# Optimization experiments

Hardware: AMD Instinct MI355X
Metric: run time of the kernel (lower is better)

Reference implementation:

```python
import jax, jax.numpy as jnp
import numpy as np

N = 20000
NEG_SLOPE = 0.2


def gat_conv(x, src, dst, W, att_src, att_dst, bias, heads, ch, concat):
    # x: [N, F_in]; src/dst: [E] (messages flow src -> dst, softmax grouped by dst)
    n = x.shape[0]
    h = (x @ W).reshape(n, heads, ch)                      # [N, H, C]
    a_s = jnp.sum(h * att_src, axis=-1)                    # [N, H]
    a_d = jnp.sum(h * att_dst, axis=-1)                    # [N, H]
    e = jax.nn.leaky_relu(a_s[src] + a_d[dst], NEG_SLOPE)  # [E, H]
    m = jax.ops.segment_max(e, dst, num_segments=n)        # segment-softmax (stable)
    ex = jnp.exp(e - m[dst])
    denom = jax.ops.segment_sum(ex, dst, num_segments=n)
    alpha = ex / (denom[dst] + 1e-16)                      # [E, H]
    msg = h[src] * alpha[:, :, None]                       # [E, H, C]
    out = jax.ops.segment_sum(msg, dst, num_segments=n)    # [N, H, C]
    out = out.reshape(n, heads * ch) if concat else out.mean(axis=1)
    return out + bias


def setup_inputs() -> dict:
    key = jax.random.key(0)
    ks = jax.random.split(key, 24)
    in_ch, h_ch, out_ch, H, OH = 512, 128, 64, 4, 6
    hid = H * h_ch  # 512
    s = 0.1
    d = {
        "x": jax.random.normal(ks[0], (N, in_ch), jnp.float32),
        "edge_index": jax.random.randint(ks[1], (2, 160000), 0, N, jnp.int32),
        "W1": jax.random.normal(ks[2], (in_ch, H * h_ch), jnp.float32) * s,
        "as1": jax.random.normal(ks[3], (1, H, h_ch), jnp.float32) * s,
        "ad1": jax.random.normal(ks[4], (1, H, h_ch), jnp.float32) * s,
        "b1": jnp.zeros((H * h_ch,), jnp.float32),
        "lW1": jax.random.normal(ks[5], (in_ch, hid), jnp.float32) * s,
        "lb1": jnp.zeros((hid,), jnp.float32),
        "W2": jax.random.normal(ks[6], (hid, H * h_ch), jnp.float32) * s,
        "as2": jax.random.normal(ks[7], (1, H, h_ch), jnp.float32) * s,
        "ad2": jax.random.normal(ks[8], (1, H, h_ch), jnp.float32) * s,
        "b2": jnp.zeros((H * h_ch,), jnp.float32),
        "lW2": jax.random.normal(ks[9], (hid, hid), jnp.float32) * s,
        "lb2": jnp.zeros((hid,), jnp.float32),
        "W3": jax.random.normal(ks[10], (hid, OH * out_ch), jnp.float32) * s,
        "as3": jax.random.normal(ks[11], (1, OH, out_ch), jnp.float32) * s,
        "ad3": jax.random.normal(ks[12], (1, OH, out_ch), jnp.float32) * s,
        "b3": jnp.zeros((out_ch,), jnp.float32),
        "lW3": jax.random.normal(ks[13], (hid, out_ch), jnp.float32) * s,
        "lb3": jnp.zeros((out_ch,), jnp.float32),
    }
    return d


def reference(x, edge_index, W1, as1, ad1, b1, lW1, lb1,
              W2, as2, ad2, b2, lW2, lb2,
              W3, as3, ad3, b3, lW3, lb3):
    n = x.shape[0]
    loops = jnp.arange(n, dtype=edge_index.dtype)  # PyG GATConv add_self_loops=True
    src = jnp.concatenate([edge_index[0], loops])
    dst = jnp.concatenate([edge_index[1], loops])
    h = jax.nn.elu(gat_conv(x, src, dst, W1, as1, ad1, b1, 4, 128, True) + x @ lW1 + lb1)
    h = jax.nn.elu(gat_conv(h, src, dst, W2, as2, ad2, b2, 4, 128, True) + h @ lW2 + lb2)
    out = gat_conv(h, src, dst, W3, as3, ad3, b3, 6, 64, False) + h @ lW3 + lb3
    return out
```

## Files before the change

### kernel.cpp

```cpp
#include <hip/hip_runtime.h>
#include <cstddef>
#include <cstdint>
#include <type_traits>

#define N_NODES 20000
#define NPAD 20096
#define E0_EDGES 160000
#define E_TOT (E0_EDGES + N_NODES)
#define CAP 64

typedef __bf16 bf16x8 __attribute__((ext_vector_type(8)));
typedef float f32x4 __attribute__((ext_vector_type(4)));

__device__ __forceinline__ ushort f2bf(float f) {
  uint32_t u = __float_as_uint(f);
  return (ushort)((u + 0x7FFFu + ((u >> 16) & 1u)) >> 16);
}
__device__ __forceinline__ float bf2f(ushort h) {
  return __uint_as_float((uint32_t)h << 16);
}

__device__ __forceinline__ int SW(int r) { return ((r >> 1) & 3) ^ ((r >> 3) & 1); }

#define GLOAD16(g, l)                                                         \
  __builtin_amdgcn_global_load_lds(                                           \
      (const __attribute__((address_space(1))) void*)(uintptr_t)(g),          \
      (__attribute__((address_space(3))) void*)(uint32_t)(uintptr_t)(l),      \
      16, 0, 0)


__global__ void fill_csr_kernel(const int* __restrict__ ei, int* __restrict__ cnt,
                                int* __restrict__ slots) {
  int e = blockIdx.x * blockDim.x + threadIdx.x;
  if (e >= E_TOT) return;
  int src, dst;
  if (e < E0_EDGES) { src = ei[e]; dst = ei[E0_EDGES + e]; }
  else              { src = e - E0_EDGES; dst = src; }
  int pos = atomicAdd(&cnt[dst], 1);
  if (pos < CAP) slots[dst * CAP + pos] = src;
}


__global__ void convert_x_kernel(const float* __restrict__ x, ushort* __restrict__ xb) {
  size_t i = ((size_t)blockIdx.x * blockDim.x + threadIdx.x) * 4;
  if (i >= (size_t)NPAD * 512) return;
  if (i < (size_t)N_NODES * 512) {
    float4 v = *(const float4*)(x + i);
    ushort4 o;
    o.x = f2bf(v.x); o.y = f2bf(v.y); o.z = f2bf(v.z); o.w = f2bf(v.w);
    *(ushort4*)(xb + i) = o;
  } else {
    *(ushort4*)(xb + i) = make_ushort4(0, 0, 0, 0);
  }
}

__global__ void transpose_all_kernel(
    const float* __restrict__ W1, const float* __restrict__ lW1,
    const float* __restrict__ W2, const float* __restrict__ lW2,
    const float* __restrict__ W3, const float* __restrict__ lW3,
    ushort* __restrict__ Bt1, ushort* __restrict__ Bt2, ushort* __restrict__ Bt3) {
  __shared__ float tile[32][33];
  const int K = 512;
  int z = blockIdx.z;
  const float* W; ushort* B; int M;
  switch (z) {
    case 0:  W = W1;  B = Bt1;              M = 512; break;
    case 1:  W = lW1; B = Bt1 + 512 * 512;  M = 512; break;
    case 2:  W = W2;  B = Bt2;              M = 512; break;
    case 3:  W = lW2; B = Bt2 + 512 * 512;  M = 512; break;
    case 4:  W = W3;  B = Bt3;              M = 384; break;
    default: W = lW3; B = Bt3 + 384 * 512;  M = 64;  break;
  }
  int mb = blockIdx.x * 32, kb = blockIdx.y * 32;
  if (mb >= M) return;
  int tx = threadIdx.x, ty = threadIdx.y;
#pragma unroll
  for (int i = 0; i < 32; i += 8)
    tile[ty + i][tx] = W[(size_t)(kb + ty + i) * M + mb + tx];
  __syncthreads();
#pragma unroll
  for (int i = 0; i < 32; i += 8)
    B[(size_t)(mb + ty + i) * K + kb + tx] = f2bf(tile[tx][ty + i]);
}


template <typename Out1T>
__global__ __launch_bounds__(256, 3) void mfma_gemm_kernel(
    const ushort* __restrict__ A,
    const ushort* __restrict__ Bt,
    ushort* __restrict__ out0, int ld0, int split,
    Out1T* __restrict__ out1, int ld1, int Mout1, const float* __restrict__ bias1,
    const float* __restrict__ att_sw, const float* __restrict__ att_dw,
    float* __restrict__ a_sp, float* __restrict__ a_dp,
    int nheads, int headC,
    int NT, int nwg) {
  const int K = 512;
  __shared__ __attribute__((aligned(16))) ushort As[3][128][32];
  __shared__ __attribute__((aligned(16))) ushort Bs[3][128][32];

  int tid = threadIdx.x, lane = tid & 63, wave = tid >> 6;
  int wrow = (wave >> 1) * 64, wcol = (wave & 1) * 64;

  size_t K2 = (size_t)K * 2;
  int rofs = lane >> 2;
  int gch = (lane & 3) ^ SW(rofs);
  int srow[2];
#pragma unroll
  for (int it = 0; it < 2; ++it) srow[it] = wave * 32 + it * 16;

  int fr = lane & 15, hi = lane >> 4;
  int rch = hi ^ SW(fr);

  char* AsB = (char*)&As[0][0][0];
  char* BsB = (char*)&Bs[0][0][0];

  int q = nwg >> 3, r = nwg & 7;

  for (int w0 = blockIdx.x; w0 < nwg; w0 += gridDim.x) {
    int xcd = w0 & 7, pos = w0 >> 3;
    int wgid = (xcd < r ? xcd * (q + 1) : r * (q + 1) + (xcd - r) * q) + pos;
    int by = wgid / NT, bx = wgid - by * NT;
    int bm = by * 128, bn = bx * 128;

    const char* pA[2];
    const char* pB[2];
#pragma unroll
    for (int it = 0; it < 2; ++it) {
      pA[it] = (const char*)A + (size_t)(bm + srow[it] + rofs) * K2 + gch * 16;
      pB[it] = (const char*)Bt + (size_t)(bn + srow[it] + rofs) * K2 + gch * 16;
    }

    f32x4 acc[4][4] = {};

#pragma unroll
    for (int s = 0; s < 2; ++s) {
#pragma unroll
      for (int it = 0; it < 2; ++it) {
        GLOAD16(pA[it], AsB + s * 8192 + srow[it] * 64);
        GLOAD16(pB[it], BsB + s * 8192 + srow[it] * 64);
      }
#pragma unroll
      for (int it = 0; it < 2; ++it) { pA[it] += 64; pB[it] += 64; }
    }

    for (int k = 0; k < 16; ++k) {
      if (k + 1 < 16) asm volatile("s_waitcnt vmcnt(4) lgkmcnt(0)" ::: "memory");
      else            asm volatile("s_waitcnt vmcnt(0) lgkmcnt(0)" ::: "memory");
      __builtin_amdgcn_s_barrier();
      asm volatile("" ::: "memory");
      if (k + 2 < 16) {
        int ss = (k + 2) % 3;
#pragma unroll
        for (int it = 0; it < 2; ++it) {
          GLOAD16(pA[it], AsB + ss * 8192 + srow[it] * 64);
          GLOAD16(pB[it], BsB + ss * 8192 + srow[it] * 64);
        }
#pragma unroll
        for (int it = 0; it < 2; ++it) { pA[it] += 64; pB[it] += 64; }
      }
      {
        int sc = k % 3;
        bf16x8 af[4], bf[4];
#pragma unroll
        for (int i = 0; i < 4; ++i)
          af[i] = *(const bf16x8*)&As[sc][wrow + i * 16 + fr][rch * 8];
#pragma unroll
        for (int j = 0; j < 4; ++j)
          bf[j] = *(const bf16x8*)&Bs[sc][wcol + j * 16 + fr][rch * 8];
#pragma unroll
        for (int i = 0; i < 4; ++i)
#pragma unroll
          for (int j = 0; j < 4; ++j)
            acc[i][j] = __builtin_amdgcn_mfma_f32_16x16x32_bf16(af[i], bf[j], acc[i][j], 0, 0, 0);
      }
      asm volatile("" ::: "memory");
    }

    asm volatile("s_waitcnt lgkmcnt(0)" ::: "memory");
    __builtin_amdgcn_s_barrier();
    asm volatile("" ::: "memory");

    int colg = bn + wcol;
    bool lower = colg < split;
    int g4 = hi << 2;
    int ccol = fr;
#pragma unroll
    for (int i = 0; i < 4; ++i) {
#pragma unroll
      for (int rr = 0; rr < 4; ++rr) {
        int row = bm + wrow + g4 + i * 16 + rr;
        if (row >= N_NODES) continue;
#pragma unroll
        for (int j = 0; j < 4; ++j) {
          int col = colg + j * 16 + ccol;
          float v = acc[i][j][rr];
          if (lower) {
            out0[(size_t)row * ld0 + col] = f2bf(v);
          } else {
            int c1 = col - split;
            if (c1 < Mout1) {
              float b = v + bias1[c1];
              if constexpr (std::is_same<Out1T, ushort>::value)
                out1[(size_t)row * ld1 + c1] = f2bf(b);
              else
                out1[(size_t)row * ld1 + c1] = b;
            }
          }
        }
      }
    }

    if (lower) {
      int hd = colg / headC;
      int cb = colg - hd * headC;
      int half = (cb >> 6) & 1;
      float ws4[4], wd4[4];
#pragma unroll
      for (int j = 0; j < 4; ++j) {
        int cc = hd * headC + cb + j * 16 + ccol;
        ws4[j] = att_sw[cc];
        wd4[j] = att_dw[cc];
      }
#pragma unroll
      for (int i = 0; i < 4; ++i) {
#pragma unroll
        for (int rr = 0; rr < 4; ++rr) {
          float ps = 0.f, pd = 0.f;
#pragma unroll
          for (int j = 0; j < 4; ++j) { ps += acc[i][j][rr] * ws4[j]; pd += acc[i][j][rr] * wd4[j]; }
#pragma unroll
          for (int o = 1; o < 16; o <<= 1) { ps += __shfl_xor(ps, o); pd += __shfl_xor(pd, o); }
          if ((lane & 15) == 0) {
            int row = bm + wrow + g4 + i * 16 + rr;
            if (row < N_NODES) {
              size_t idx = ((size_t)row * nheads + hd) * 2;
              if (headC == 128) {
                a_sp[idx + half] = ps;
                a_dp[idx + half] = pd;
              } else {
                a_sp[idx] = ps;  a_sp[idx + 1] = 0.f;
                a_dp[idx] = pd;  a_dp[idx + 1] = 0.f;
              }
            }
          }
        }
      }
    }
  }
}


template <int H, int C>
__global__ __launch_bounds__(128) void gather12_fused(
    const int* __restrict__ cnt, const int* __restrict__ slots,
    const float* __restrict__ a_sp, const float* __restrict__ a_dp,
    const ushort* __restrict__ hbuf, const float* __restrict__ gat_bias,
    const ushort* __restrict__ skip_in, ushort* __restrict__ outbuf) {
  __shared__ float al[H][CAP];
  __shared__ int srcs[CAP];
  int n = blockIdx.x;
  int t = threadIdx.x, lane = t & 63, w = t >> 6;
  int deg = min(cnt[n], CAP);

  int sj = 0;
  if (lane < deg) sj = slots[n * CAP + lane];
#pragma unroll
  for (int hh = 0; hh < 2; ++hh) {
    int hd = 2 * w + hh;
    float e = -1e30f;
    if (lane < deg) {
      size_t is = ((size_t)sj * H + hd) * 2;
      size_t id = ((size_t)n * H + hd) * 2;
      float v = a_sp[is] + a_sp[is + 1] + a_dp[id] + a_dp[id + 1];
      e = v > 0.f ? v : 0.2f * v;
    }
    float m = e;
#pragma unroll
    for (int o = 32; o > 0; o >>= 1) m = fmaxf(m, __shfl_xor(m, o));
    float ex = (lane < deg) ? expf(e - m) : 0.f;
    float s = ex;
#pragma unroll
    for (int o = 32; o > 0; o >>= 1) s += __shfl_xor(s, o);
    float inv = 1.f / (s + 1e-16f);
    if (lane < deg) al[hd][lane] = ex * inv;
  }
  if (w == 0 && lane < deg) srcs[lane] = sj;
  __syncthreads();

  int f0 = 4 * t, hd = t >> 5;
  float a0 = 0.f, a1 = 0.f, a2 = 0.f, a3 = 0.f;
  for (int j = 0; j < deg; ++j) {
    float a = al[hd][j];
    ushort4 hv = *(const ushort4*)(hbuf + (size_t)srcs[j] * (H * C) + f0);
    a0 += a * bf2f(hv.x);
    a1 += a * bf2f(hv.y);
    a2 += a * bf2f(hv.z);
    a3 += a * bf2f(hv.w);
  }
  ushort4 sk = *(const ushort4*)(skip_in + (size_t)n * (H * C) + f0);
  float o0 = a0 + gat_bias[f0 + 0] + bf2f(sk.x);
  float o1 = a1 + gat_bias[f0 + 1] + bf2f(sk.y);
  float o2 = a2 + gat_bias[f0 + 2] + bf2f(sk.z);
  float o3 = a3 + gat_bias[f0 + 3] + bf2f(sk.w);
  o0 = o0 > 0.f ? o0 : (expf(o0) - 1.f);
  o1 = o1 > 0.f ? o1 : (expf(o1) - 1.f);
  o2 = o2 > 0.f ? o2 : (expf(o2) - 1.f);
  o3 = o3 > 0.f ? o3 : (expf(o3) - 1.f);
  ushort4 ov;
  ov.x = f2bf(o0); ov.y = f2bf(o1); ov.z = f2bf(o2); ov.w = f2bf(o3);
  *(ushort4*)(outbuf + (size_t)n * (H * C) + f0) = ov;
}


__global__ __launch_bounds__(128) void gather3_fused(
    const int* __restrict__ cnt, const int* __restrict__ slots,
    const float* __restrict__ a_sp, const float* __restrict__ a_dp,
    const ushort* __restrict__ hbuf , const float* __restrict__ b3,
    float* __restrict__ out ) {
  __shared__ float al[6][CAP];
  __shared__ int srcs[CAP];
  __shared__ float part[2][64];
  int n = blockIdx.x;
  int t = threadIdx.x, lane = t & 63, w = t >> 6;
  int deg = min(cnt[n], CAP);

  int sj = 0;
  if (lane < deg) sj = slots[n * CAP + lane];
#pragma unroll
  for (int hh = 0; hh < 3; ++hh) {
    int hd = 3 * w + hh;
    float e = -1e30f;
    if (lane < deg) {
      size_t is = ((size_t)sj * 6 + hd) * 2;
      size_t id = ((size_t)n * 6 + hd) * 2;
      float v = a_sp[is] + a_sp[is + 1] + a_dp[id] + a_dp[id + 1];
      e = v > 0.f ? v : 0.2f * v;
    }
    float m = e;
#pragma unroll
    for (int o = 32; o > 0; o >>= 1) m = fmaxf(m, __shfl_xor(m, o));
    float ex = (lane < deg) ? expf(e - m) : 0.f;
    float s = ex;
#pragma unroll
    for (int o = 32; o > 0; o >>= 1) s += __shfl_xor(s, o);
    float inv = (1.f / 6.f) / (s + 1e-16f);
    if (lane < deg) al[hd][lane] = ex * inv;
  }
  if (w == 0 && lane < deg) srcs[lane] = sj;
  __syncthreads();

  int c = t & 63;
  float acc = 0.f;
  for (int j = w; j < deg; j += 2) {
    const ushort* hr = hbuf + (size_t)srcs[j] * 384 + c;
#pragma unroll
    for (int hd = 0; hd < 6; ++hd) acc += al[hd][j] * bf2f(hr[hd * 64]);
  }
  part[w][c] = acc;
  __syncthreads();
  if (t < 64) {
    size_t oi = (size_t)n * 64 + t;
    out[oi] += part[0][t] + part[1][t] + b3[t];
  }
}


extern "C" void kernel_launch(void* const* d_in, const int* in_sizes, int n_in,
                              void* d_out, int out_size, void* d_ws, size_t ws_size,
                              hipStream_t stream) {
  const float* x   = (const float*)d_in[0];
  const int*   ei  = (const int*)d_in[1];
  const float* W1  = (const float*)d_in[2];
  const float* as1 = (const float*)d_in[3];
  const float* ad1 = (const float*)d_in[4];
  const float* b1  = (const float*)d_in[5];
  const float* lW1 = (const float*)d_in[6];
  const float* lb1 = (const float*)d_in[7];
  const float* W2  = (const float*)d_in[8];
  const float* as2 = (const float*)d_in[9];
  const float* ad2 = (const float*)d_in[10];
  const float* b2  = (const float*)d_in[11];
  const float* lW2 = (const float*)d_in[12];
  const float* lb2 = (const float*)d_in[13];
  const float* W3  = (const float*)d_in[14];
  const float* as3 = (const float*)d_in[15];
  const float* ad3 = (const float*)d_in[16];
  const float* b3  = (const float*)d_in[17];
  const float* lW3 = (const float*)d_in[18];
  const float* lb3 = (const float*)d_in[19];
  float* out = (float*)d_out;

  char* ws = (char*)d_ws;
  auto alloc = [&](size_t bytes) -> void* {
    void* p = (void*)ws;
    ws += (bytes + 255) & ~(size_t)255;
    return p;
  };
  ushort* xb    = (ushort*)alloc((size_t)NPAD * 512 * 2);
  ushort* Pb    = (ushort*)alloc((size_t)NPAD * 512 * 2);
  ushort* Qb    = (ushort*)alloc((size_t)NPAD * 512 * 2);
  ushort* skipb = (ushort*)alloc((size_t)N_NODES * 512 * 2);
  ushort* hb    = (ushort*)alloc((size_t)N_NODES * 512 * 2);
  ushort* Bt1   = (ushort*)alloc((size_t)1024 * 512 * 2);
  ushort* Bt2   = (ushort*)alloc((size_t)1024 * 512 * 2);
  ushort* Bt3   = (ushort*)alloc((size_t)512 * 512 * 2);
  float*  a_sp  = (float*)alloc((size_t)N_NODES * 6 * 2 * 4);
  float*  a_dp  = (float*)alloc((size_t)N_NODES * 6 * 2 * 4);
  int*    cnt   = (int*)alloc((size_t)N_NODES * 4);
  int*    slots = (int*)alloc((size_t)N_NODES * CAP * 4);

  hipMemsetAsync(cnt, 0, N_NODES * sizeof(int), stream);
  fill_csr_kernel<<<(E_TOT + 255) / 256, 256, 0, stream>>>(ei, cnt, slots);

  convert_x_kernel<<<((NPAD * 512 / 4) + 255) / 256, 256, 0, stream>>>(x, xb);
  transpose_all_kernel<<<dim3(16, 16, 6), dim3(32, 8), 0, stream>>>(
      W1, lW1, W2, lW2, W3, lW3, Bt1, Bt2, Bt3);

  const int NBY = NPAD / 128;
  const int NWG12 = NBY * 8;
  const int NWG3  = NBY * 4;
  const int PERSIST = 256 * 3;
  const int G12 = NWG12 < PERSIST ? NWG12 : PERSIST;
  const int G3  = NWG3  < PERSIST ? NWG3  : PERSIST;

  mfma_gemm_kernel<ushort><<<G12, 256, 0, stream>>>(
      xb, Bt1, hb, 512, 512, skipb, 512, 512, lb1, as1, ad1, a_sp, a_dp, 4, 128,
      8, NWG12);
  gather12_fused<4, 128><<<N_NODES, 128, 0, stream>>>(cnt, slots, a_sp, a_dp, hb, b1, skipb, Pb);

  mfma_gemm_kernel<ushort><<<G12, 256, 0, stream>>>(
      Pb, Bt2, hb, 512, 512, skipb, 512, 512, lb2, as2, ad2, a_sp, a_dp, 4, 128,
      8, NWG12);
  gather12_fused<4, 128><<<N_NODES, 128, 0, stream>>>(cnt, slots, a_sp, a_dp, hb, b2, skipb, Qb);

  mfma_gemm_kernel<float><<<G3, 256, 0, stream>>>(
      Qb, Bt3, hb, 384, 384, out, 64, 64, lb3, as3, ad3, a_sp, a_dp, 6, 64,
      4, NWG3);
  gather3_fused<<<N_NODES, 128, 0, stream>>>(cnt, slots, a_sp, a_dp, hb, b3, out);
}
```

Before: 259.0 us.

## Load B fragments directly from global memory, drop B shared staging

New measurement: 325.0 us. 25.5% more time.

```diff
diff --git a/kernel.cpp b/kernel.cpp
--- a/kernel.cpp
+++ b/kernel.cpp
@@ -85,7 +85,7 @@
 
 
 template <typename Out1T>
-__global__ __launch_bounds__(256, 3) void mfma_gemm_kernel(
+__global__ __launch_bounds__(256, 4) void mfma_gemm_kernel(
     const ushort* __restrict__ A,
     const ushort* __restrict__ Bt,
     ushort* __restrict__ out0, int ld0, int split,
@@ -96,7 +96,6 @@
     int NT, int nwg) {
   const int K = 512;
   __shared__ __attribute__((aligned(16))) ushort As[3][128][32];
-  __shared__ __attribute__((aligned(16))) ushort Bs[3][128][32];
 
   int tid = threadIdx.x, lane = tid & 63, wave = tid >> 6;
   int wrow = (wave >> 1) * 64, wcol = (wave & 1) * 64;
@@ -112,7 +111,6 @@
   int rch = hi ^ SW(fr);
 
   char* AsB = (char*)&As[0][0][0];
-  char* BsB = (char*)&Bs[0][0][0];
 
   int q = nwg >> 3, r = nwg & 7;
 
@@ -123,50 +121,50 @@
     int bm = by * 128, bn = bx * 128;
 
     const char* pA[2];
-    const char* pB[2];
-#pragma unroll
-    for (int it = 0; it < 2; ++it) {
+#pragma unroll
+    for (int it = 0; it < 2; ++it)
       pA[it] = (const char*)A + (size_t)(bm + srow[it] + rofs) * K2 + gch * 16;
-      pB[it] = (const char*)Bt + (size_t)(bn + srow[it] + rofs) * K2 + gch * 16;
-    }
+    const char* pBf[4];
+#pragma unroll
+    for (int j = 0; j < 4; ++j)
+      pBf[j] = (const char*)Bt + (size_t)(bn + wcol + j * 16 + fr) * K2 + hi * 16;
 
     f32x4 acc[4][4] = {};
 
 #pragma unroll
     for (int s = 0; s < 2; ++s) {
 #pragma unroll
-      for (int it = 0; it < 2; ++it) {
+      for (int it = 0; it < 2; ++it)
         GLOAD16(pA[it], AsB + s * 8192 + srow[it] * 64);
-        GLOAD16(pB[it], BsB + s * 8192 + srow[it] * 64);
-      }
-#pragma unroll
-      for (int it = 0; it < 2; ++it) { pA[it] += 64; pB[it] += 64; }
-    }
-
+#pragma unroll
+      for (int it = 0; it < 2; ++it) pA[it] += 64;
+    }
+
+#pragma unroll
     for (int k = 0; k < 16; ++k) {
-      if (k + 1 < 16) asm volatile("s_waitcnt vmcnt(4) lgkmcnt(0)" ::: "memory");
-      else            asm volatile("s_waitcnt vmcnt(0) lgkmcnt(0)" ::: "memory");
+      if (k < 15) asm volatile("s_waitcnt vmcnt(2) lgkmcnt(0)" ::: "memory");
+      else        asm volatile("s_waitcnt vmcnt(0) lgkmcnt(0)" ::: "memory");
       __builtin_amdgcn_s_barrier();
+      asm volatile("" ::: "memory");
+      bf16x8 bf[4];
+#pragma unroll
+      for (int j = 0; j < 4; ++j)
+        bf[j] = *(const bf16x8*)(pBf[j] + k * 64);
       asm volatile("" ::: "memory");
       if (k + 2 < 16) {
         int ss = (k + 2) % 3;
 #pragma unroll
-        for (int it = 0; it < 2; ++it) {
+        for (int it = 0; it < 2; ++it)
           GLOAD16(pA[it], AsB + ss * 8192 + srow[it] * 64);
-          GLOAD16(pB[it], BsB + ss * 8192 + srow[it] * 64);
-        }
-#pragma unroll
-        for (int it = 0; it < 2; ++it) { pA[it] += 64; pB[it] += 64; }
+#pragma unroll
+        for (int it = 0; it < 2; ++it) pA[it] += 64;
       }
       {
         int sc = k % 3;
-        bf16x8 af[4], bf[4];
+        bf16x8 af[4];
 #pragma unroll
         for (int i = 0; i < 4; ++i)
           af[i] = *(const bf16x8*)&As[sc][wrow + i * 16 + fr][rch * 8];
-#pragma unroll
-        for (int j = 0; j < 4; ++j)
-          bf[j] = *(const bf16x8*)&Bs[sc][wcol + j * 16 + fr][rch * 8];
 #pragma unroll
         for (int i = 0; i < 4; ++i)
 #pragma unroll
@@ -419,7 +417,7 @@
   const int NBY = NPAD / 128;
   const int NWG12 = NBY * 8;
   const int NWG3  = NBY * 4;
-  const int PERSIST = 256 * 3;
+  const int PERSIST = 256 * 4;
   const int G12 = NWG12 < PERSIST ? NWG12 : PERSIST;
   const int G3  = NWG3  < PERSIST ? NWG3  : PERSIST;
 
```
